# Performance work log

Measured on AMD Instinct MI355X. Metric: run time of the kernel, lower is better.

## Reference

```python
import jax, jax.numpy as jnp
import numpy as np

B, S, D, N, H, K = 32, 512, 2048, 16, 128, 64
EPS = 1e-6


def setup_inputs() -> dict:
    key = jax.random.key(0)
    ks = jax.random.split(key, 8)
    # glorot-uniform-like scale for the (D, N, H) attention kernels
    kern_scale = (6.0 / (D + H)) ** 0.5
    down_sd = 1.0 / K  # matches module: mean 0, sd = 1/downsampling_k
    q = jax.random.normal(ks[0], (B, S, D), dtype=jnp.float32)
    k = jax.random.normal(ks[1], (B, S, D), dtype=jnp.float32)
    v = jax.random.normal(ks[2], (B, S, D), dtype=jnp.float32)
    query_kernel = jax.random.uniform(ks[3], (D, N, H), jnp.float32, -kern_scale, kern_scale)
    key_kernel = jax.random.uniform(ks[4], (D, N, H), jnp.float32, -kern_scale, kern_scale)
    value_kernel = jax.random.uniform(ks[5], (D, N, H), jnp.float32, -kern_scale, kern_scale)
    key_down = down_sd * jax.random.normal(ks[6], (K, S), dtype=jnp.float32)
    value_down = down_sd * jax.random.normal(ks[7], (K, S), dtype=jnp.float32)
    return dict(q=q, k=k, v=v, query_kernel=query_kernel, key_kernel=key_kernel,
                value_kernel=value_kernel, key_down=key_down, value_down=value_down)


def reference(q, k, v, query_kernel, key_kernel, value_kernel, key_down, value_down):
    # Linformer-style downsampling of keys/values along the sequence axis: [B,S,D] -> [B,K,D]
    key_ds = jnp.einsum('ks,bsd->bkd', key_down, k)
    val_ds = jnp.einsum('ks,bsd->bkd', value_down, v)
    # Per-head projections
    queries = jnp.einsum('bqd,dnh->bqnh', q, query_kernel)   # [B,S,N,H]
    keys = jnp.einsum('bkd,dnh->bknh', key_ds, key_kernel)   # [B,K,N,H]
    values = jnp.einsum('bkd,dnh->bknh', val_ds, value_kernel)  # [B,K,N,H]
    # Kernelized linear attention with elu+1 feature map (mask=False branch)
    phi_q = jax.nn.elu(queries) + 1.0
    phi_k = jax.nn.elu(keys) + 1.0
    s = jnp.einsum('bknd,bknh->bndh', phi_k, values)  # [B,N,H,H]
    z = jnp.sum(phi_k, axis=1)                        # [B,N,H]
    qs = jnp.einsum('bqnd,bndh->bqnh', phi_q, s)      # [B,S,N,H]
    qz = jnp.einsum('bqnd,bnd->bqn', phi_q, z) + EPS  # [B,S,N]
    a_v = qs / qz[..., None]
    return a_v.reshape(B, S, N * H)
```

## Files before the change

### kernel.cpp

```cpp
#include <hip/hip_runtime.h>
#include <cstdint>
#include <cstddef>

typedef float f32x4 __attribute__((ext_vector_type(4)));
typedef short s16x8 __attribute__((ext_vector_type(8)));
typedef unsigned short u16;

#define EPS 1e-6f

__device__ __forceinline__ u16 f2bf(float f) {
    unsigned u = __float_as_uint(f);
    u += 0x7FFFu + ((u >> 16) & 1u);
    return (u16)(u >> 16);
}
__device__ __forceinline__ float bf2f(u16 u) {
    return __uint_as_float(((unsigned)u) << 16);
}

typedef const __attribute__((address_space(1))) void cg_void;
typedef __attribute__((address_space(3))) void l_void;
__device__ __forceinline__ void async16(void* dst_lds, const void* src_g) {
    __builtin_amdgcn_global_load_lds((cg_void*)src_g, (l_void*)dst_lds, 16, 0, 0);
}

#define BARRIER() do { asm volatile("" ::: "memory"); \
                       __builtin_amdgcn_s_barrier();  \
                       asm volatile("" ::: "memory"); } while (0)

__global__ __launch_bounds__(256) void prep(
    const float* __restrict__ q, u16* __restrict__ qb,
    const float* __restrict__ w0, const float* __restrict__ w1,
    const float* __restrict__ w2, u16* __restrict__ o0,
    u16* __restrict__ o1, u16* __restrict__ o2)
{
    int bid = blockIdx.x;
    if (bid < 12288) {
        int which = bid >> 12;
        int t = bid & 4095;
        const float* in = which == 0 ? w0 : which == 1 ? w1 : w2;
        u16* out        = which == 0 ? o0 : which == 1 ? o1 : o2;
        int bx = (t & 63) * 32, by = (t >> 6) * 32;
        __shared__ u16 tl[32][33];
        int tx = threadIdx.x & 31, ty = threadIdx.x >> 5;
        for (int i = ty; i < 32; i += 8)
            tl[i][tx] = f2bf(in[(size_t)(by + i) * 2048 + bx + tx]);
        __syncthreads();
        for (int i = ty; i < 32; i += 8)
            out[(size_t)(bx + i) * 2048 + by + tx] = tl[tx][i];
    } else {
        int cb = bid - 12288;
        size_t base = (size_t)cb * 256 + threadIdx.x;
        #pragma unroll
        for (int it = 0; it < 8; ++it) {
            size_t i = base + (size_t)it * 1048576;
            float4 f = ((const float4*)q)[i];
            ushort4 o;
            o.x = f2bf(f.x); o.y = f2bf(f.y); o.z = f2bf(f.z); o.w = f2bf(f.w);
            ((ushort4*)qb)[i] = o;
        }
    }
}

__global__ __launch_bounds__(256) void down_mfma(
    const float* __restrict__ kin, const float* __restrict__ vin,
    const float* __restrict__ wdk, const float* __restrict__ wdv,
    u16* __restrict__ kds, u16* __restrict__ vds)
{
    const float* x  = blockIdx.z ? vin : kin;
    const float* wd = blockIdx.z ? wdv : wdk;
    u16* outp       = blockIdx.z ? vds : kds;
    int b = blockIdx.y, d0 = blockIdx.x * 128;
    __shared__ __align__(16) u16 At[64 * 32];
    __shared__ __align__(16) u16 Bt[128 * 40];
    int tid = threadIdx.x;
    int w = tid >> 6, l = tid & 63, l16 = l & 15, k8 = l >> 4;
    f32x4 acc[4][2] = {};
    for (int s0 = 0; s0 < 512; s0 += 32) {
        __syncthreads();
        for (int c = tid; c < 512; c += 256) {
            int kkr = c >> 3, sc = (c & 7) << 2;
            float4 f = *(const float4*)&wd[kkr * 512 + s0 + sc];
            u16* dst = &At[kkr * 32 + sc];
            dst[0] = f2bf(f.x); dst[1] = f2bf(f.y); dst[2] = f2bf(f.z); dst[3] = f2bf(f.w);
        }
        for (int c = tid; c < 512; c += 256) {
            int sp = c >> 5, dq = (c & 31) << 2;
            int srow = sp << 1;
            const float* xp = &x[((size_t)(b * 512) + s0 + srow) * 2048 + d0 + dq];
            float4 f0 = *(const float4*)xp;
            float4 f1 = *(const float4*)(xp + 2048);
            unsigned p0 = (unsigned)f2bf(f0.x) | ((unsigned)f2bf(f1.x) << 16);
            unsigned p1 = (unsigned)f2bf(f0.y) | ((unsigned)f2bf(f1.y) << 16);
            unsigned p2 = (unsigned)f2bf(f0.z) | ((unsigned)f2bf(f1.z) << 16);
            unsigned p3 = (unsigned)f2bf(f0.w) | ((unsigned)f2bf(f1.w) << 16);
            *(unsigned*)&Bt[(dq + 0) * 40 + srow] = p0;
            *(unsigned*)&Bt[(dq + 1) * 40 + srow] = p1;
            *(unsigned*)&Bt[(dq + 2) * 40 + srow] = p2;
            *(unsigned*)&Bt[(dq + 3) * 40 + srow] = p3;
        }
        __syncthreads();
        s16x8 af[4], bfr[2];
        #pragma unroll
        for (int fm = 0; fm < 4; ++fm)
            af[fm] = *(const s16x8*)&At[(fm * 16 + l16) * 32 + k8 * 8];
        #pragma unroll
        for (int fn = 0; fn < 2; ++fn)
            bfr[fn] = *(const s16x8*)&Bt[(w * 32 + fn * 16 + l16) * 40 + k8 * 8];
        #pragma unroll
        for (int fm = 0; fm < 4; ++fm)
            #pragma unroll
            for (int fn = 0; fn < 2; ++fn)
                acc[fm][fn] = __builtin_amdgcn_mfma_f32_16x16x32_bf16(af[fm], bfr[fn], acc[fm][fn], 0, 0, 0);
    }
    #pragma unroll
    for (int fm = 0; fm < 4; ++fm)
        #pragma unroll
        for (int fn = 0; fn < 2; ++fn)
            #pragma unroll
            for (int j = 0; j < 4; ++j) {
                int r = fm * 16 + k8 * 4 + j;
                int c = w * 32 + fn * 16 + l16;
                outp[((size_t)(b * 64 + r)) * 2048 + d0 + c] = f2bf(acc[fm][fn][j]);
            }
}

__global__ __launch_bounds__(512, 2) void gemm256_elu(
    const u16* __restrict__ A, const u16* __restrict__ BT,
    u16* __restrict__ C, int M, int N, int K)
{
    __shared__ __align__(16) u16 lds[8][8192];
    const int tid = threadIdx.x;
    const int w = tid >> 6, l = tid & 63;
    const int wm = w >> 2, wn = w & 3;
    const int l16 = l & 15, k8 = l >> 4;
    const int NT = K >> 6;

    const int nbn = N >> 8;
    const int nwg = gridDim.x;
    int wg = blockIdx.x;
    if ((nwg & 7) == 0) wg = (wg & 7) * (nwg >> 3) + (wg >> 3);
    const int row0 = (wg / nbn) << 8, col0 = (wg % nbn) << 8;

    const int lr  = l >> 3;
    const int scb = (((l & 7) ^ lr) << 4);
    const int swzr = (l16 & 7) << 4;

#define PANEL(s, m, h) (&lds[((s) << 2) | ((m) << 1) | (h)][0])

#define STG(pan, G, prow0, kk0) do {                                             \
        _Pragma("unroll")                                                        \
        for (int i_ = 0; i_ < 2; ++i_) {                                         \
            int seg_ = w + (i_ << 3);                                            \
            const u16* src_ = (G) + (size_t)((prow0) + (seg_ << 3) + lr) * K     \
                              + (kk0) + (scb >> 1);                              \
            async16((pan) + (seg_ << 9), src_);                                  \
        } } while (0)

#define LDA(slot, mh) do { const u16* p_ = PANEL(slot, 0, mh);                   \
        _Pragma("unroll")                                                        \
        for (int fm_ = 0; fm_ < 4; ++fm_)                                        \
        _Pragma("unroll")                                                        \
        for (int ks_ = 0; ks_ < 2; ++ks_)                                        \
            Af[fm_][ks_] = *(const s16x8*)(p_ + (wm * 64 + fm_ * 16 + l16) * 64  \
                           + (((ks_ * 64 + k8 * 16) ^ swzr) >> 1)); } while (0)

#define LDB(slot, nh, dst) do { const u16* p_ = PANEL(slot, 1, nh);              \
        _Pragma("unroll")                                                        \
        for (int fn_ = 0; fn_ < 2; ++fn_)                                        \
        _Pragma("unroll")                                                        \
        for (int ks_ = 0; ks_ < 2; ++ks_)                                        \
            dst[fn_][ks_] = *(const s16x8*)(p_ + (wn * 32 + fn_ * 16 + l16) * 64 \
                           + (((ks_ * 64 + k8 * 16) ^ swzr) >> 1)); } while (0)

#define MM(mh, nh, BF) do {                                                      \
        __builtin_amdgcn_s_setprio(1);                                           \
        _Pragma("unroll")                                                        \
        for (int fm_ = 0; fm_ < 4; ++fm_)                                        \
        _Pragma("unroll")                                                        \
        for (int fn_ = 0; fn_ < 2; ++fn_)                                        \
        _Pragma("unroll")                                                        \
        for (int ks_ = 0; ks_ < 2; ++ks_)                                        \
            acc[mh][nh][fm_][fn_] = __builtin_amdgcn_mfma_f32_16x16x32_bf16(     \
                Af[fm_][ks_], BF[fn_][ks_], acc[mh][nh][fm_][fn_], 0, 0, 0);     \
        __builtin_amdgcn_s_setprio(0); } while (0)

    f32x4 acc[2][2][4][2] = {};
    s16x8 Af[4][2], Bf0[2][2], Bf1[2][2];

    STG(PANEL(0, 0, 0), A,  row0,       0);
    STG(PANEL(0, 1, 0), BT, col0,       0);
    STG(PANEL(0, 1, 1), BT, col0 + 128, 0);
    STG(PANEL(0, 0, 1), A,  row0 + 128, 0);
    if (NT > 1) {
        STG(PANEL(1, 0, 0), A,  row0,       64);
        STG(PANEL(1, 1, 0), BT, col0,       64);
        STG(PANEL(1, 1, 1), BT, col0 + 128, 64);
        asm volatile("s_waitcnt vmcnt(6)" ::: "memory");
    } else {
        asm volatile("s_waitcnt vmcnt(0)" ::: "memory");
    }
    BARRIER();

    int cur = 0;
    for (int t = 0; t < NT; ++t) {
        const int nxt = cur ^ 1;
        LDA(cur, 0);
        LDB(cur, 0, Bf0);
        if (t + 1 < NT) STG(PANEL(nxt, 0, 1), A, row0 + 128, (t + 1) << 6);
        BARRIER();
        MM(0, 0, Bf0);
        BARRIER();
        LDB(cur, 1, Bf1);
        if (t + 2 < NT) STG(PANEL(cur, 0, 0), A, row0, (t + 2) << 6);
        BARRIER();
        MM(0, 1, Bf1);
        BARRIER();
        LDA(cur, 1);
        if (t + 2 < NT) STG(PANEL(cur, 1, 0), BT, col0, (t + 2) << 6);
        BARRIER();
        MM(1, 1, Bf1);
        BARRIER();
        if (t + 2 < NT) STG(PANEL(cur, 1, 1), BT, col0 + 128, (t + 2) << 6);
        BARRIER();
        MM(1, 0, Bf0);
        if (t == NT - 2)      asm volatile("s_waitcnt vmcnt(0)" ::: "memory");
        else if (t < NT - 2)  asm volatile("s_waitcnt vmcnt(6)" ::: "memory");
        BARRIER();
        cur = nxt;
    }
#undef PANEL
#undef STG
#undef LDA
#undef LDB
#undef MM

    #pragma unroll
    for (int mh = 0; mh < 2; ++mh)
        #pragma unroll
        for (int fm = 0; fm < 4; ++fm)
            #pragma unroll
            for (int j = 0; j < 4; ++j) {
                int r = row0 + mh * 128 + wm * 64 + fm * 16 + k8 * 4 + j;
                size_t rb = (size_t)r * N;
                #pragma unroll
                for (int nh = 0; nh < 2; ++nh)
                    #pragma unroll
                    for (int fn = 0; fn < 2; ++fn) {
                        int c = col0 + nh * 128 + wn * 32 + fn * 16 + l16;
                        float x = acc[mh][nh][fm][fn][j];
                        x = x > 0.0f ? x + 1.0f : __expf(x);
                        C[rb + c] = f2bf(x);
                    }
            }
}

__global__ __launch_bounds__(256) void gemm128_dual(
    const u16* __restrict__ A0, const u16* __restrict__ B0, u16* __restrict__ C0,
    const u16* __restrict__ A1, const u16* __restrict__ B1, u16* __restrict__ C1)
{
    const u16* A  = blockIdx.z ? A1 : A0;
    const u16* BT = blockIdx.z ? B1 : B0;
    u16* C        = blockIdx.z ? C1 : C0;
    const bool elu = (blockIdx.z == 0);
    const int K = 2048;

    __shared__ __align__(16) u16 lds[2][8192];
    const int tid = threadIdx.x;
    const int w = tid >> 6, l = tid & 63;
    const int wm = w >> 1, wn = w & 1;
    const int l16 = l & 15, k8 = l >> 4;
    const int sr = (w << 4) + (l >> 2);
    const int sc = (l & 3) << 3;
    const int row0 = blockIdx.y * 128, col0 = blockIdx.x * 128;
    const int nk = K >> 5;
    f32x4 acc[4][4] = {};

#define STAGE(buf, kt) do {                                                        \
        int kk0 = (kt) << 5;                                                       \
        _Pragma("unroll")                                                          \
        for (int i = 0; i < 2; ++i) {                                              \
            const u16* ga = A + (size_t)(row0 + i * 64 + sr) * K + kk0 + sc;       \
            async16(&lds[buf][i * 2048 + (w << 9)], ga);                           \
            const u16* gb = BT + (size_t)(col0 + i * 64 + sr) * K + kk0 + sc;      \
            async16(&lds[buf][4096 + i * 2048 + (w << 9)], gb);                    \
        }                                                                          \
    } while (0)

    STAGE(0, 0);
    asm volatile("s_waitcnt vmcnt(0)" ::: "memory");
    __syncthreads();
    int cur = 0;
    for (int kt = 0; kt < nk; ++kt) {
        if (kt + 1 < nk) STAGE(cur ^ 1, kt + 1);
        s16x8 af[4], bfr[4];
        const u16* Ab = &lds[cur][0];
        const u16* Bb = &lds[cur][4096];
        #pragma unroll
        for (int fm = 0; fm < 4; ++fm)
            af[fm] = *(const s16x8*)&Ab[((wm << 6) + (fm << 4) + l16) * 32 + (k8 << 3)];
        #pragma unroll
        for (int fn = 0; fn < 4; ++fn)
            bfr[fn] = *(const s16x8*)&Bb[((wn << 6) + (fn << 4) + l16) * 32 + (k8 << 3)];
        #pragma unroll
        for (int fm = 0; fm < 4; ++fm)
            #pragma unroll
            for (int fn = 0; fn < 4; ++fn)
                acc[fm][fn] = __builtin_amdgcn_mfma_f32_16x16x32_bf16(af[fm], bfr[fn], acc[fm][fn], 0, 0, 0);
        __syncthreads();
        cur ^= 1;
    }
#undef STAGE

    #pragma unroll
    for (int fm = 0; fm < 4; ++fm)
        #pragma unroll
        for (int j = 0; j < 4; ++j) {
            int r = row0 + (wm << 6) + (fm << 4) + (k8 << 2) + j;
            size_t rbase = (size_t)r * 2048;
            #pragma unroll
            for (int fn = 0; fn < 4; ++fn) {
                int c = col0 + (wn << 6) + (fn << 4) + l16;
                float x = acc[fm][fn][j];
                if (elu) x = x > 0.0f ? x + 1.0f : __expf(x);
                C[rbase + c] = f2bf(x);
            }
        }
}

__global__ __launch_bounds__(256) void sz_kernel(
    const u16* __restrict__ phik, const u16* __restrict__ vals,
    u16* __restrict__ sT, float* __restrict__ z)
{
    int b = blockIdx.x >> 4, n = blockIdx.x & 15;
    __shared__ __align__(16) u16 pk[64 * 128];
    __shared__ __align__(16) u16 vv[64 * 128];
    int tid = threadIdx.x;
    for (int i = tid; i < 1024; i += 256) {
        int r = i >> 4, c8 = (i & 15) << 3;
        size_t g = ((size_t)(b * 64 + r)) * 2048 + n * 128 + c8;
        ((s16x8*)pk)[i] = *(const s16x8*)&phik[g];
        ((s16x8*)vv)[i] = *(const s16x8*)&vals[g];
    }
    __syncthreads();
    if (tid < 128) {
        float s = 0.0f;
        for (int kk = 0; kk < 64; ++kk) s += bf2f(pk[kk * 128 + tid]);
        z[((size_t)(b * 16 + n)) * 128 + tid] = s;
    }
    int hg = tid >> 4, dg = tid & 15;
    int h0 = hg * 8, d0 = dg * 8;
    float acc[8][8] = {};
    for (int kk = 0; kk < 64; ++kk) {
        s16x8 vr = *(const s16x8*)&vv[kk * 128 + h0];
        s16x8 pr = *(const s16x8*)&pk[kk * 128 + d0];
        float va[8], pa[8];
        #pragma unroll
        for (int i = 0; i < 8; ++i) { va[i] = bf2f((u16)vr[i]); pa[i] = bf2f((u16)pr[i]); }
        #pragma unroll
        for (int i = 0; i < 8; ++i)
            #pragma unroll
            for (int j = 0; j < 8; ++j)
                acc[i][j] += va[i] * pa[j];
    }
    size_t base = ((size_t)(b * 16 + n)) * 16384;
    #pragma unroll
    for (int i = 0; i < 8; ++i) {
        u16 row[8];
        #pragma unroll
        for (int j = 0; j < 8; ++j) row[j] = f2bf(acc[i][j]);
        *(s16x8*)&sT[base + (size_t)(h0 + i) * 128 + d0] = *(s16x8*)row;
    }
}

__global__ __launch_bounds__(256) void qs_kernel(
    const u16* __restrict__ phiq, const u16* __restrict__ sT,
    const float* __restrict__ z, float* __restrict__ out)
{
    const int gb = blockIdx.x;
    const int rb = gb & 3, bn = gb >> 2;
    const int b = bn >> 4, n = bn & 15;
    __shared__ __align__(16) u16 Blds[128 * 128];
    const int tid = threadIdx.x;
    const int w = tid >> 6, l = tid & 63;
    const int l16 = l & 15, k8 = l >> 4;

    {
        const u16* base = sT + (size_t)bn * 16384;
        #pragma unroll
        for (int r0 = 0; r0 < 128; r0 += 16) {
            int row = r0 + (w << 2) + (l >> 4);
            int scb = (((l & 15) ^ (row & 7)) << 4);
            async16(&Blds[(r0 + (w << 2)) * 128], base + (size_t)row * 128 + (scb >> 1));
        }
    }

    const size_t arow0 = (size_t)(b * 512 + rb * 128);
    s16x8 Af[2][4];
    #pragma unroll
    for (int fm = 0; fm < 2; ++fm)
        #pragma unroll
        for (int ks = 0; ks < 4; ++ks) {
            int row = (w << 5) + (fm << 4) + l16;
            Af[fm][ks] = *(const s16x8*)(phiq + (arow0 + row) * 2048 + n * 128
                                         + (ks << 5) + (k8 << 3));
        }

    s16x8 Bz[4];
    #pragma unroll
    for (int ks = 0; ks < 4; ++ks) {
        const float* zp = z + (size_t)bn * 128 + (ks << 5) + (k8 << 3);
        float4 f0 = *(const float4*)zp;
        float4 f1 = *(const float4*)(zp + 4);
        u16 tmp[8] = { f2bf(f0.x), f2bf(f0.y), f2bf(f0.z), f2bf(f0.w),
                       f2bf(f1.x), f2bf(f1.y), f2bf(f1.z), f2bf(f1.w) };
        Bz[ks] = *(const s16x8*)tmp;
    }

    f32x4 accz[2] = {};
    #pragma unroll
    for (int fm = 0; fm < 2; ++fm)
        #pragma unroll
        for (int ks = 0; ks < 4; ++ks)
            accz[fm] = __builtin_amdgcn_mfma_f32_16x16x32_bf16(Af[fm][ks], Bz[ks], accz[fm], 0, 0, 0);

    asm volatile("s_waitcnt vmcnt(0)" ::: "memory");
    BARRIER();

    const int swz = (l16 & 7) << 4;
    f32x4 acc[2][8] = {};
    #pragma unroll
    for (int fn = 0; fn < 8; ++fn) {
        s16x8 Bf[4];
        #pragma unroll
        for (int ks = 0; ks < 4; ++ks)
            Bf[ks] = *(const s16x8*)&Blds[((fn << 4) + l16) * 128
                                          + ((((ks << 6) + (k8 << 4)) ^ swz) >> 1)];
        #pragma unroll
        for (int fm = 0; fm < 2; ++fm)
            #pragma unroll
            for (int ks = 0; ks < 4; ++ks)
                acc[fm][fn] = __builtin_amdgcn_mfma_f32_16x16x32_bf16(Af[fm][ks], Bf[ks], acc[fm][fn], 0, 0, 0);
    }

    #pragma unroll
    for (int fm = 0; fm < 2; ++fm)
        #pragma unroll
        for (int j = 0; j < 4; ++j) {
            int row = (w << 5) + (fm << 4) + (k8 << 2) + j;
            float rq = 1.0f / (accz[fm][j] + EPS);
            size_t ob = (arow0 + row) * 2048 + n * 128;
            #pragma unroll
            for (int fn = 0; fn < 8; ++fn)
                out[ob + (fn << 4) + l16] = acc[fm][fn][j] * rq;
        }
}

extern "C" void kernel_launch(void* const* d_in, const int* in_sizes, int n_in,
                              void* d_out, int out_size, void* d_ws, size_t ws_size,
                              hipStream_t stream) {
    (void)in_sizes; (void)n_in; (void)out_size; (void)ws_size;
    const float* q   = (const float*)d_in[0];
    const float* k   = (const float*)d_in[1];
    const float* v   = (const float*)d_in[2];
    const float* wq  = (const float*)d_in[3];
    const float* wk  = (const float*)d_in[4];
    const float* wv  = (const float*)d_in[5];
    const float* kdw = (const float*)d_in[6];
    const float* vdw = (const float*)d_in[7];
    float* out = (float*)d_out;

    char* p = (char*)d_ws;
    u16* qb   = (u16*)p; p += (size_t)16384 * 2048 * 2;
    u16* wqT  = (u16*)p; p += (size_t)2048 * 2048 * 2;
    u16* wkT  = (u16*)p; p += (size_t)2048 * 2048 * 2;
    u16* wvT  = (u16*)p; p += (size_t)2048 * 2048 * 2;
    u16* kds  = (u16*)p; p += (size_t)2048 * 2048 * 2;
    u16* vds  = (u16*)p; p += (size_t)2048 * 2048 * 2;
    u16* phiq = (u16*)p; p += (size_t)16384 * 2048 * 2;
    u16* phik = (u16*)p; p += (size_t)2048 * 2048 * 2;
    u16* vals = (u16*)p; p += (size_t)2048 * 2048 * 2;
    u16* sT   = (u16*)p; p += (size_t)512 * 128 * 128 * 2;
    float* z  = (float*)p; p += (size_t)512 * 128 * 4;

    prep<<<16384, 256, 0, stream>>>(q, qb, wq, wk, wv, wqT, wkT, wvT);
    down_mfma<<<dim3(16, 32, 2), 256, 0, stream>>>(k, v, kdw, vdw, kds, vds);
    gemm128_dual<<<dim3(16, 16, 2), 256, 0, stream>>>(kds, wkT, phik, vds, wvT, vals);
    gemm256_elu<<<512, 512, 0, stream>>>(qb, wqT, phiq, 16384, 2048, 2048);
    sz_kernel<<<512, 256, 0, stream>>>(phik, vals, sT, z);
    qs_kernel<<<2048, 256, 0, stream>>>(phiq, sT, z, out);
}
```

Measured before the change: 383.2 us.

## Merge prep and downsample kernels; prefetch next B fragment in GEMM loop

The prep (bf16 cast and weight transpose) and the Linformer downsampling MFMA kernel are merged into one launch. Downsample blocks come first so they overlap with the memory-bound conversion blocks. Separately, the main Q-projection GEMM loop is unrolled by two with ping-pong B fragment registers. The first B fragment of the next tile is now loaded from LDS at the end of the current tile, hiding LDS latency before the first MFMA group. The costs are more shared memory per block in the merged kernel, more registers in the GEMM, and an unroll that assumes NT is even and at least 2.

After: 372.3 us. 2.8% less time.

```diff
diff --git a/kernel.cpp b/kernel.cpp
--- a/kernel.cpp
+++ b/kernel.cpp
@@ -27,29 +27,92 @@
                        __builtin_amdgcn_s_barrier();  \
                        asm volatile("" ::: "memory"); } while (0)
 
-__global__ __launch_bounds__(256) void prep(
+__global__ __launch_bounds__(256) void prep_down(
     const float* __restrict__ q, u16* __restrict__ qb,
     const float* __restrict__ w0, const float* __restrict__ w1,
     const float* __restrict__ w2, u16* __restrict__ o0,
-    u16* __restrict__ o1, u16* __restrict__ o2)
+    u16* __restrict__ o1, u16* __restrict__ o2,
+    const float* __restrict__ kin, const float* __restrict__ vin,
+    const float* __restrict__ wdk, const float* __restrict__ wdv,
+    u16* __restrict__ kds, u16* __restrict__ vds)
 {
-    int bid = blockIdx.x;
-    if (bid < 12288) {
-        int which = bid >> 12;
-        int t = bid & 4095;
+    __shared__ __align__(16) u16 At[64 * 32];
+    __shared__ __align__(16) u16 Bt[128 * 40];
+    __shared__ u16 tl[32][33];
+    const int bid = blockIdx.x;
+    const int tid = threadIdx.x;
+
+    if (bid < 1024) {
+        const int sel = bid >> 9, rem = bid & 511;
+        const int b = rem >> 4, d0 = (rem & 15) << 7;
+        const float* x  = sel ? vin : kin;
+        const float* wd = sel ? wdv : wdk;
+        u16* outp       = sel ? vds : kds;
+        int w = tid >> 6, l = tid & 63, l16 = l & 15, k8 = l >> 4;
+        f32x4 acc[4][2] = {};
+        for (int s0 = 0; s0 < 512; s0 += 32) {
+            __syncthreads();
+            for (int c = tid; c < 512; c += 256) {
+                int kkr = c >> 3, sc = (c & 7) << 2;
+                float4 f = *(const float4*)&wd[kkr * 512 + s0 + sc];
+                u16* dst = &At[kkr * 32 + sc];
+                dst[0] = f2bf(f.x); dst[1] = f2bf(f.y); dst[2] = f2bf(f.z); dst[3] = f2bf(f.w);
+            }
+            for (int c = tid; c < 512; c += 256) {
+                int sp = c >> 5, dq = (c & 31) << 2;
+                int srow = sp << 1;
+                const float* xp = &x[((size_t)(b * 512) + s0 + srow) * 2048 + d0 + dq];
+                float4 f0 = *(const float4*)xp;
+                float4 f1 = *(const float4*)(xp + 2048);
+                unsigned p0 = (unsigned)f2bf(f0.x) | ((unsigned)f2bf(f1.x) << 16);
+                unsigned p1 = (unsigned)f2bf(f0.y) | ((unsigned)f2bf(f1.y) << 16);
+                unsigned p2 = (unsigned)f2bf(f0.z) | ((unsigned)f2bf(f1.z) << 16);
+                unsigned p3 = (unsigned)f2bf(f0.w) | ((unsigned)f2bf(f1.w) << 16);
+                *(unsigned*)&Bt[(dq + 0) * 40 + srow] = p0;
+                *(unsigned*)&Bt[(dq + 1) * 40 + srow] = p1;
+                *(unsigned*)&Bt[(dq + 2) * 40 + srow] = p2;
+                *(unsigned*)&Bt[(dq + 3) * 40 + srow] = p3;
+            }
+            __syncthreads();
+            s16x8 af[4], bfr[2];
+            #pragma unroll
+            for (int fm = 0; fm < 4; ++fm)
+                af[fm] = *(const s16x8*)&At[(fm * 16 + l16) * 32 + k8 * 8];
+            #pragma unroll
+            for (int fn = 0; fn < 2; ++fn)
+                bfr[fn] = *(const s16x8*)&Bt[(w * 32 + fn * 16 + l16) * 40 + k8 * 8];
+            #pragma unroll
+            for (int fm = 0; fm < 4; ++fm)
+                #pragma unroll
+                for (int fn = 0; fn < 2; ++fn)
+                    acc[fm][fn] = __builtin_amdgcn_mfma_f32_16x16x32_bf16(af[fm], bfr[fn], acc[fm][fn], 0, 0, 0);
+        }
+        #pragma unroll
+        for (int fm = 0; fm < 4; ++fm)
+            #pragma unroll
+            for (int fn = 0; fn < 2; ++fn)
+                #pragma unroll
+                for (int j = 0; j < 4; ++j) {
+                    int r = fm * 16 + k8 * 4 + j;
+                    int c = w * 32 + fn * 16 + l16;
+                    outp[((size_t)(b * 64 + r)) * 2048 + d0 + c] = f2bf(acc[fm][fn][j]);
+                }
+    } else if (bid < 13312) {
+        int wb = bid - 1024;
+        int which = wb >> 12;
+        int t = wb & 4095;
         const float* in = which == 0 ? w0 : which == 1 ? w1 : w2;
         u16* out        = which == 0 ? o0 : which == 1 ? o1 : o2;
         int bx = (t & 63) * 32, by = (t >> 6) * 32;
-        __shared__ u16 tl[32][33];
-        int tx = threadIdx.x & 31, ty = threadIdx.x >> 5;
+        int tx = tid & 31, ty = tid >> 5;
         for (int i = ty; i < 32; i += 8)
             tl[i][tx] = f2bf(in[(size_t)(by + i) * 2048 + bx + tx]);
         __syncthreads();
         for (int i = ty; i < 32; i += 8)
             out[(size_t)(bx + i) * 2048 + by + tx] = tl[tx][i];
     } else {
-        int cb = bid - 12288;
-        size_t base = (size_t)cb * 256 + threadIdx.x;
+        int cb = bid - 13312;
+        size_t base = (size_t)cb * 256 + tid;
         #pragma unroll
         for (int it = 0; it < 8; ++it) {
             size_t i = base + (size_t)it * 1048576;
@@ -59,69 +122,6 @@
             ((ushort4*)qb)[i] = o;
         }
     }
-}
-
-__global__ __launch_bounds__(256) void down_mfma(
-    const float* __restrict__ kin, const float* __restrict__ vin,
-    const float* __restrict__ wdk, const float* __restrict__ wdv,
-    u16* __restrict__ kds, u16* __restrict__ vds)
-{
-    const float* x  = blockIdx.z ? vin : kin;
-    const float* wd = blockIdx.z ? wdv : wdk;
-    u16* outp       = blockIdx.z ? vds : kds;
-    int b = blockIdx.y, d0 = blockIdx.x * 128;
-    __shared__ __align__(16) u16 At[64 * 32];
-    __shared__ __align__(16) u16 Bt[128 * 40];
-    int tid = threadIdx.x;
-    int w = tid >> 6, l = tid & 63, l16 = l & 15, k8 = l >> 4;
-    f32x4 acc[4][2] = {};
-    for (int s0 = 0; s0 < 512; s0 += 32) {
-        __syncthreads();
-        for (int c = tid; c < 512; c += 256) {
-            int kkr = c >> 3, sc = (c & 7) << 2;
-            float4 f = *(const float4*)&wd[kkr * 512 + s0 + sc];
-            u16* dst = &At[kkr * 32 + sc];
-            dst[0] = f2bf(f.x); dst[1] = f2bf(f.y); dst[2] = f2bf(f.z); dst[3] = f2bf(f.w);
-        }
-        for (int c = tid; c < 512; c += 256) {
-            int sp = c >> 5, dq = (c & 31) << 2;
-            int srow = sp << 1;
-            const float* xp = &x[((size_t)(b * 512) + s0 + srow) * 2048 + d0 + dq];
-            float4 f0 = *(const float4*)xp;
-            float4 f1 = *(const float4*)(xp + 2048);
-            unsigned p0 = (unsigned)f2bf(f0.x) | ((unsigned)f2bf(f1.x) << 16);
-            unsigned p1 = (unsigned)f2bf(f0.y) | ((unsigned)f2bf(f1.y) << 16);
-            unsigned p2 = (unsigned)f2bf(f0.z) | ((unsigned)f2bf(f1.z) << 16);
-            unsigned p3 = (unsigned)f2bf(f0.w) | ((unsigned)f2bf(f1.w) << 16);
-            *(unsigned*)&Bt[(dq + 0) * 40 + srow] = p0;
-            *(unsigned*)&Bt[(dq + 1) * 40 + srow] = p1;
-            *(unsigned*)&Bt[(dq + 2) * 40 + srow] = p2;
-            *(unsigned*)&Bt[(dq + 3) * 40 + srow] = p3;
-        }
-        __syncthreads();
-        s16x8 af[4], bfr[2];
-        #pragma unroll
-        for (int fm = 0; fm < 4; ++fm)
-            af[fm] = *(const s16x8*)&At[(fm * 16 + l16) * 32 + k8 * 8];
-        #pragma unroll
-        for (int fn = 0; fn < 2; ++fn)
-            bfr[fn] = *(const s16x8*)&Bt[(w * 32 + fn * 16 + l16) * 40 + k8 * 8];
-        #pragma unroll
-        for (int fm = 0; fm < 4; ++fm)
-            #pragma unroll
-            for (int fn = 0; fn < 2; ++fn)
-                acc[fm][fn] = __builtin_amdgcn_mfma_f32_16x16x32_bf16(af[fm], bfr[fn], acc[fm][fn], 0, 0, 0);
-    }
-    #pragma unroll
-    for (int fm = 0; fm < 4; ++fm)
-        #pragma unroll
-        for (int fn = 0; fn < 2; ++fn)
-            #pragma unroll
-            for (int j = 0; j < 4; ++j) {
-                int r = fm * 16 + k8 * 4 + j;
-                int c = w * 32 + fn * 16 + l16;
-                outp[((size_t)(b * 64 + r)) * 2048 + d0 + c] = f2bf(acc[fm][fn][j]);
-            }
 }
 
 __global__ __launch_bounds__(512, 2) void gemm256_elu(
@@ -184,55 +184,52 @@
                 Af[fm_][ks_], BF[fn_][ks_], acc[mh][nh][fm_][fn_], 0, 0, 0);     \
         __builtin_amdgcn_s_setprio(0); } while (0)
 
+#define TILE(t, cur, nxt, BFc, BFn) do {                                         \
+                                                                        \
+        LDA(cur, 0);                                                             \
+        if ((t) + 1 < NT) STG(PANEL(nxt, 0, 1), A, row0 + 128, ((t) + 1) << 6);  \
+        BARRIER(); MM(0, 0, BFc); BARRIER();                                     \
+                                                                        \
+        LDB(cur, 1, Bf1);                                                        \
+        if ((t) + 2 < NT) STG(PANEL(cur, 0, 0), A, row0, ((t) + 2) << 6);        \
+        BARRIER(); MM(0, 1, Bf1); BARRIER();                                     \
+                                                                        \
+        LDA(cur, 1);                                                             \
+        if ((t) + 2 < NT) STG(PANEL(cur, 1, 0), BT, col0, ((t) + 2) << 6);       \
+        BARRIER(); MM(1, 1, Bf1); BARRIER();                                     \
+                                                                        \
+        if ((t) + 2 < NT) STG(PANEL(cur, 1, 1), BT, col0 + 128, ((t) + 2) << 6); \
+        BARRIER(); MM(1, 0, BFc);                                                \
+        if ((t) == NT - 2)     asm volatile("s_waitcnt vmcnt(0)" ::: "memory");  \
+        else if ((t) < NT - 2) asm volatile("s_waitcnt vmcnt(6)" ::: "memory");  \
+        BARRIER();                                                               \
+        if ((t) + 1 < NT) LDB(nxt, 0, BFn);       \
+    } while (0)
+
     f32x4 acc[2][2][4][2] = {};
-    s16x8 Af[4][2], Bf0[2][2], Bf1[2][2];
+    s16x8 Af[4][2], Bf0a[2][2], Bf0b[2][2], Bf1[2][2];
 
     STG(PANEL(0, 0, 0), A,  row0,       0);
     STG(PANEL(0, 1, 0), BT, col0,       0);
     STG(PANEL(0, 1, 1), BT, col0 + 128, 0);
     STG(PANEL(0, 0, 1), A,  row0 + 128, 0);
-    if (NT > 1) {
-        STG(PANEL(1, 0, 0), A,  row0,       64);
-        STG(PANEL(1, 1, 0), BT, col0,       64);
-        STG(PANEL(1, 1, 1), BT, col0 + 128, 64);
-        asm volatile("s_waitcnt vmcnt(6)" ::: "memory");
-    } else {
-        asm volatile("s_waitcnt vmcnt(0)" ::: "memory");
-    }
+    STG(PANEL(1, 0, 0), A,  row0,       64);
+    STG(PANEL(1, 1, 0), BT, col0,       64);
+    STG(PANEL(1, 1, 1), BT, col0 + 128, 64);
+    asm volatile("s_waitcnt vmcnt(6)" ::: "memory");
     BARRIER();
-
-    int cur = 0;
-    for (int t = 0; t < NT; ++t) {
-        const int nxt = cur ^ 1;
-        LDA(cur, 0);
-        LDB(cur, 0, Bf0);
-        if (t + 1 < NT) STG(PANEL(nxt, 0, 1), A, row0 + 128, (t + 1) << 6);
-        BARRIER();
-        MM(0, 0, Bf0);
-        BARRIER();
-        LDB(cur, 1, Bf1);
-        if (t + 2 < NT) STG(PANEL(cur, 0, 0), A, row0, (t + 2) << 6);
-        BARRIER();
-        MM(0, 1, Bf1);
-        BARRIER();
-        LDA(cur, 1);
-        if (t + 2 < NT) STG(PANEL(cur, 1, 0), BT, col0, (t + 2) << 6);
-        BARRIER();
-        MM(1, 1, Bf1);
-        BARRIER();
-        if (t + 2 < NT) STG(PANEL(cur, 1, 1), BT, col0 + 128, (t + 2) << 6);
-        BARRIER();
-        MM(1, 0, Bf0);
-        if (t == NT - 2)      asm volatile("s_waitcnt vmcnt(0)" ::: "memory");
-        else if (t < NT - 2)  asm volatile("s_waitcnt vmcnt(6)" ::: "memory");
-        BARRIER();
-        cur = nxt;
+    LDB(0, 0, Bf0a);
+
+    for (int t = 0; t < NT; t += 2) {
+        TILE(t,     0, 1, Bf0a, Bf0b);
+        TILE(t + 1, 1, 0, Bf0b, Bf0a);
     }
 #undef PANEL
 #undef STG
 #undef LDA
 #undef LDB
 #undef MM
+#undef TILE
 
     #pragma unroll
     for (int mh = 0; mh < 2; ++mh)
@@ -482,8 +479,8 @@
     u16* sT   = (u16*)p; p += (size_t)512 * 128 * 128 * 2;
     float* z  = (float*)p; p += (size_t)512 * 128 * 4;
 
-    prep<<<16384, 256, 0, stream>>>(q, qb, wq, wk, wv, wqT, wkT, wvT);
-    down_mfma<<<dim3(16, 32, 2), 256, 0, stream>>>(k, v, kdw, vdw, kds, vds);
+    prep_down<<<17408, 256, 0, stream>>>(q, qb, wq, wk, wv, wqT, wkT, wvT,
+                                         k, v, kdw, vdw, kds, vds);
     gemm128_dual<<<dim3(16, 16, 2), 256, 0, stream>>>(kds, wkT, phik, vds, wvT, vals);
     gemm256_elu<<<512, 512, 0, stream>>>(qb, wqT, phiq, 16384, 2048, 2048);
     sz_kernel<<<512, 256, 0, stream>>>(phik, vals, sT, z);
```
